# Kernel tuning notes

Measured on AMD Instinct MI355X. Metric: run time of the kernel, lower is better.

The kernel has to match this reference:

```python
import jax, jax.numpy as jnp
import numpy as np

LN_EPS = 1e-5
MASK_FILL = -1e9


def setup_inputs() -> dict:
    key = jax.random.key(0)
    ks = jax.random.split(key, 10)
    B, L, D, H, O, K = 128, 2048, 128, 256, 128, 64
    return {
        "sequence_emb": jax.random.normal(ks[0], (B, L, D), jnp.float32),
        "mask": jax.random.randint(ks[1], (B, L), 0, 2, jnp.int32),
        "target_emb": jax.random.normal(ks[2], (B, D), jnp.float32),
        "pos_table": jax.random.normal(ks[3], (10000, D), jnp.float32) * 0.02,
        "W_imp1": jax.random.normal(ks[4], (3 * D, H), jnp.float32) * (1.0 / np.sqrt(3 * D)),
        "b_imp1": jnp.zeros((H,), jnp.float32),
        "W_imp2": jax.random.normal(ks[5], (H, 1), jnp.float32) * (1.0 / np.sqrt(H)),
        "b_imp2": jnp.zeros((1,), jnp.float32),
        "W_enc1": jax.random.normal(ks[6], (2 * D, H), jnp.float32) * (1.0 / np.sqrt(2 * D)),
        "b_enc1": jnp.zeros((H,), jnp.float32),
        "W_enc2": jax.random.normal(ks[7], (H, O), jnp.float32) * (1.0 / np.sqrt(H)),
        "b_enc2": jnp.zeros((O,), jnp.float32),
        "ln_gamma": jnp.ones((O,), jnp.float32),
        "ln_beta": jnp.zeros((O,), jnp.float32),
        "top_k": K,
    }


def reference(sequence_emb, mask, target_emb, pos_table, W_imp1, b_imp1, W_imp2,
              b_imp2, W_enc1, b_enc1, W_enc2, b_enc2, ln_gamma, ln_beta, top_k):
    B, L, D = sequence_emb.shape
    # position embedding lookup (positions identical across batch -> keep (L,D) and broadcast)
    positions = jnp.minimum(jnp.arange(L), pos_table.shape[0] - 1)
    pos_emb = jnp.broadcast_to(pos_table[positions][None], (B, L, D))
    combined = jnp.concatenate([sequence_emb, pos_emb], axis=-1)          # (B,L,2D)
    tgt = jnp.broadcast_to(target_emb[:, None, :], (B, L, D))
    imp_in = jnp.concatenate([combined, tgt], axis=-1)                    # (B,L,3D)
    # importance MLP -> scalar score per event
    h = jax.nn.relu(imp_in @ W_imp1 + b_imp1)
    scores = (h @ W_imp2 + b_imp2)[..., 0]                                # (B,L)
    scores = jnp.where(mask == 0, MASK_FILL, scores)
    # masked top-k, then gather in chronological (sorted-index) order
    topk_values, topk_indices = jax.lax.top_k(scores, top_k)              # (B,K)
    idx_sorted = jnp.sort(topk_indices, axis=-1)
    sel = jnp.take_along_axis(combined, idx_sorted[..., None], axis=1)    # (B,K,2D)
    encoded = jax.nn.relu(sel @ W_enc1 + b_enc1) @ W_enc2 + b_enc2        # (B,K,O)
    # reorder scores to match sorted index order (torch: gather by argsort of indices)
    order = jnp.argsort(topk_indices, axis=-1)
    topk_scores = jnp.take_along_axis(topk_values, order, axis=-1)
    attn = jax.nn.softmax(topk_scores, axis=-1)                           # (B,K)
    pooled = jnp.einsum('bk,bkd->bd', attn, encoded)                      # (B,O)
    mu = jnp.mean(pooled, axis=-1, keepdims=True)
    var = jnp.var(pooled, axis=-1, keepdims=True)
    return (pooled - mu) * jax.lax.rsqrt(var + LN_EPS) * ln_gamma + ln_beta
```

## Files before the change

### kernel.cpp

```cpp
#include <hip/hip_runtime.h>
#include <hip/hip_bf16.h>

namespace {
constexpr int NB = 128;
constexpr int NL = 2048;
constexpr int ND = 128;
constexpr int NH = 256;
constexpr int NO = 128;
constexpr int NK = 64;
constexpr int MCAP = 192;
constexpr int HTHR = 96;
constexpr int BLOOP = 8;
constexpr float MASK_FILL_F = -1e9f;
constexpr float LN_EPS_F = 1e-5f;
}

typedef __attribute__((ext_vector_type(8))) short bf16x8;
typedef __attribute__((ext_vector_type(4))) float f32x4;

__device__ __forceinline__ unsigned short bf16rne(float x) {
  unsigned u = __float_as_uint(x);
  return (unsigned short)((u + 0x7FFFu + ((u >> 16) & 1u)) >> 16);
}

__global__ __launch_bounds__(256) void k_prep(
    const float* __restrict__ W1, const float* __restrict__ pos,
    const float* __restrict__ tgt, const float* __restrict__ b1,
    const float* __restrict__ We1, const float* __restrict__ We2,
    unsigned short* __restrict__ W1aT, float* __restrict__ P,
    float* __restrict__ T, unsigned short* __restrict__ We1T,
    unsigned short* __restrict__ We2T) {
  const int blk = blockIdx.x, t = threadIdx.x;
  if (blk < ND) {
    W1aT[(size_t)t * ND + blk] = bf16rne(W1[(size_t)blk * NH + t]);
    return;
  }
  if (blk >= ND + NL + NB) {
    const int b2 = blk - (ND + NL + NB);
    if (b2 < 256) {
      We1T[(size_t)t * 256 + b2] = bf16rne(We1[(size_t)b2 * NH + t]);
    } else {
      const int d = b2 - 256;
      if (t < NO) We2T[(size_t)t * 256 + d] = bf16rne(We2[(size_t)d * NO + t]);
    }
    return;
  }
  int r, w_off, add_bias;
  const float* src;
  float* out;
  if (blk < ND + NL) {
    r = blk - ND; src = pos; out = P; w_off = ND; add_bias = 1;
  } else {
    r = blk - (ND + NL); src = tgt; out = T; w_off = 2 * ND; add_bias = 0;
  }
  __shared__ float row[ND];
  if (t < ND) row[t] = src[(size_t)r * ND + t];
  __syncthreads();
  float acc = add_bias ? b1[t] : 0.0f;
#pragma unroll 8
  for (int d = 0; d < ND; ++d)
    acc = fmaf(row[d], W1[(size_t)(w_off + d) * NH + t], acc);
  out[(size_t)r * NH + t] = acc;
}

__global__ __launch_bounds__(512, 2) void k_scores_mfma(
    const float* __restrict__ seq, const int* __restrict__ mask,
    const unsigned short* __restrict__ W1aT, const float* __restrict__ w2,
    const float* __restrict__ b2, const float* __restrict__ b1,
    const float* __restrict__ T, float* __restrict__ scores) {
  const int l0 = blockIdx.x * 128;
  const int b0 = blockIdx.y * BLOOP;
  const int t = threadIdx.x;
  const int lane = t & 63;
  const int w = t >> 6;
  const int wh = w & 3;
  const int wl = w >> 2;
  const int lh = lane & 15;
  const int kq = lane >> 4;

  __shared__ unsigned short sSeq[2][128 * 128];
  __shared__ float sRed[4][128];

  bf16x8 a[4][4];
#pragma unroll
  for (int ks = 0; ks < 4; ++ks)
#pragma unroll
    for (int mt = 0; mt < 4; ++mt)
      a[ks][mt] = *(const bf16x8*)(
          W1aT + (size_t)(wh * 64 + mt * 16 + lh) * ND + ks * 32 + kq * 8);

  float4 wv[4], b1v[4];
#pragma unroll
  for (int mt = 0; mt < 4; ++mt) {
    wv[mt] = *(const float4*)(w2 + wh * 64 + mt * 16 + kq * 4);
    b1v[mt] = *(const float4*)(b1 + wh * 64 + mt * 16 + kq * 4);
  }
  const float b2v = b2[0];

  ushort4 pf[8];
  auto prefetch = [&](int bb) {
    const float4* g = (const float4*)(seq + ((size_t)bb * NL + l0) * ND);
#pragma unroll
    for (int i = 0; i < 8; ++i) {
      const float4 f = g[t + i * 512];
      pf[i].x = bf16rne(f.x); pf[i].y = bf16rne(f.y);
      pf[i].z = bf16rne(f.z); pf[i].w = bf16rne(f.w);
    }
  };
  auto commit = [&](unsigned short* dst) {
#pragma unroll
    for (int i = 0; i < 8; ++i) {
      const int v = t + i * 512;
      const int row = v >> 5;
      const int c8 = (v & 31) * 8;
      const int off = (row << 8) + (c8 ^ ((row & 15) << 4));
      *(ushort4*)((char*)dst + off) = pf[i];
    }
  };

  prefetch(b0);
  commit((unsigned short*)sSeq[0]);
  __syncthreads();

#pragma unroll 1
  for (int j = 0; j < BLOOP; ++j) {
    const int b = b0 + j;
    unsigned short* cSeq = (unsigned short*)sSeq[j & 1];
    unsigned short* nSeq = (unsigned short*)sSeq[(j & 1) ^ 1];

    if (j + 1 < BLOOP) prefetch(b + 1);

    float4 Tv[4];
#pragma unroll
    for (int mt = 0; mt < 4; ++mt)
      Tv[mt] = *(const float4*)(T + (size_t)b * NH + wh * 64 + mt * 16 + kq * 4);

    f32x4 acc[4][4];
#pragma unroll
    for (int mt = 0; mt < 4; ++mt)
#pragma unroll
      for (int nt = 0; nt < 4; ++nt) acc[mt][nt] = (f32x4){0.f, 0.f, 0.f, 0.f};

#pragma unroll
    for (int ks = 0; ks < 4; ++ks) {
      bf16x8 Bf[4];
#pragma unroll
      for (int nt = 0; nt < 4; ++nt) {
        const int row = wl * 64 + nt * 16 + lh;
        const int off = (row << 8) + (((ks << 6) + (kq << 4)) ^ ((row & 15) << 4));
        Bf[nt] = *(const bf16x8*)((const char*)cSeq + off);
      }
#pragma unroll
      for (int mt = 0; mt < 4; ++mt)
#pragma unroll
        for (int nt = 0; nt < 4; ++nt)
          acc[mt][nt] = __builtin_amdgcn_mfma_f32_16x16x32_bf16(
              a[ks][mt], Bf[nt], acc[mt][nt], 0, 0, 0);
    }
    __syncthreads();
    if (j + 1 < BLOOP) commit(nSeq);

    float p[4] = {0.f, 0.f, 0.f, 0.f};
#pragma unroll
    for (int mt = 0; mt < 4; ++mt) {
#pragma unroll
      for (int nt = 0; nt < 4; ++nt) {
        float z;
        z = acc[mt][nt][0] + Tv[mt].x + b1v[mt].x; p[nt] = fmaf(fmaxf(z, 0.f), wv[mt].x, p[nt]);
        z = acc[mt][nt][1] + Tv[mt].y + b1v[mt].y; p[nt] = fmaf(fmaxf(z, 0.f), wv[mt].y, p[nt]);
        z = acc[mt][nt][2] + Tv[mt].z + b1v[mt].z; p[nt] = fmaf(fmaxf(z, 0.f), wv[mt].z, p[nt]);
        z = acc[mt][nt][3] + Tv[mt].w + b1v[mt].w; p[nt] = fmaf(fmaxf(z, 0.f), wv[mt].w, p[nt]);
      }
    }
#pragma unroll
    for (int nt = 0; nt < 4; ++nt) {
      float v = p[nt];
      v += __shfl_xor(v, 16);
      v += __shfl_xor(v, 32);
      if (lane < 16) sRed[wh][wl * 64 + nt * 16 + lane] = v;
    }
    __syncthreads();
    if (t < 128) {
      const int l = l0 + t;
      float sc = sRed[0][t] + sRed[1][t] + sRed[2][t] + sRed[3][t] + b2v;
      if (mask[(size_t)b * NL + l] == 0) sc = MASK_FILL_F;
      scores[(size_t)b * NL + l] = sc;
    }
  }
}

__global__ __launch_bounds__(1024, 4) void k_topA(
    const float* __restrict__ scores, int* __restrict__ cand_idx,
    int* __restrict__ cand_n) {
  const int b = blockIdx.x, t = threadIdx.x;
  __shared__ unsigned hist[4096];
  __shared__ unsigned chunk[256];
  __shared__ unsigned suf[257];
  __shared__ int sCsel, sBsel;
  __shared__ unsigned sCntHi, sCntB;
  __shared__ int s_cand[MCAP];

  const unsigned mkey = ~__float_as_uint(MASK_FILL_F);
  for (int i = t; i < 4096; i += 1024) hist[i] = 0;
  if (t == 0) { sCntHi = 0; sCntB = 0; sCsel = 0; suf[256] = 0; }
  __syncthreads();
  unsigned key2[2];
#pragma unroll
  for (int i = 0; i < 2; ++i) {
    unsigned u = __float_as_uint(scores[(size_t)b * NL + t + i * 1024]);
    u = (u & 0x80000000u) ? ~u : (u | 0x80000000u);
    key2[i] = u;
    if (u != mkey) atomicAdd(&hist[u >> 20], 1u);
  }
  __syncthreads();
  if (t < 256) {
    unsigned s = 0;
#pragma unroll 4
    for (int j = 0; j < 16; ++j) s += hist[t * 16 + j];
    chunk[t] = s;
  }
  __syncthreads();
  if (t < 256) {
    unsigned s = 0;
    for (int j = t; j < 256; ++j) s += chunk[j];
    suf[t] = s;
    if (s >= (unsigned)HTHR) atomicMax(&sCsel, t);
  }
  __syncthreads();
  const int c = sCsel;
  if (t == 0) sBsel = c * 16;
  __syncthreads();
  if (t < 16) {
    unsigned s = 0;
    for (int j = c * 16 + t; j < c * 16 + 16; ++j) s += hist[j];
    if (s + suf[c + 1] >= (unsigned)HTHR) atomicMax(&sBsel, c * 16 + t);
  }
  __syncthreads();
  const unsigned B = (unsigned)sBsel;
#pragma unroll
  for (int i = 0; i < 2; ++i) {
    if (key2[i] != mkey && (key2[i] >> 20) > B) {
      unsigned pos_ = atomicAdd(&sCntHi, 1u);
      s_cand[pos_] = t + i * 1024;
    }
  }
  __syncthreads();
  const unsigned hi = sCntHi;
#pragma unroll
  for (int i = 0; i < 2; ++i) {
    if (key2[i] != mkey && (key2[i] >> 20) == B) {
      unsigned pos_ = atomicAdd(&sCntB, 1u);
      if (hi + pos_ < (unsigned)MCAP) s_cand[hi + pos_] = t + i * 1024;
    }
  }
  __syncthreads();
  unsigned n = sCntHi + sCntB;
  if (n > (unsigned)MCAP) n = MCAP;
  if (t < MCAP) cand_idx[(size_t)b * MCAP + t] = (t < (int)n) ? s_cand[t] : 0;
  if (t == 0) cand_n[b] = (int)n;
}

__global__ __launch_bounds__(256) void k_rescoreW(
    const float* __restrict__ seq, const int* __restrict__ mask,
    const float* __restrict__ W1, const float* __restrict__ w2,
    const float* __restrict__ b2, const float* __restrict__ P,
    const float* __restrict__ T, const int* __restrict__ cand_idx,
    const int* __restrict__ cand_n, float* __restrict__ cscore) {
  const int b = blockIdx.y;
  const int s0 = blockIdx.x * 32;
  const int n = cand_n[b];
  if (s0 >= n) return;
  const int t = threadIdx.x;
  __shared__ float s_seq[32 * 128];
  __shared__ int s_l[32];
  if (t < 32) {
    const int slot = s0 + t;
    s_l[t] = (slot < n) ? cand_idx[(size_t)b * MCAP + slot] : 0;
  }
  __syncthreads();
#pragma unroll
  for (int i = 0; i < 4; ++i) {
    const int v = t + i * 256;
    const int r = v >> 5, c = v & 31;
    ((float4*)s_seq)[r * 32 + c] =
        ((const float4*)(seq + ((size_t)b * NL + s_l[r]) * ND))[c];
  }
  __syncthreads();

  const int hg = t & 63, rg = t >> 6;
  float acc[8][4];
#pragma unroll
  for (int r = 0; r < 8; ++r)
#pragma unroll
    for (int j = 0; j < 4; ++j) acc[r][j] = 0.0f;

  const float4* Wp = (const float4*)W1;
  for (int d0 = 0; d0 < ND; d0 += 4) {
    float4 wq[4];
#pragma unroll
    for (int j = 0; j < 4; ++j) wq[j] = Wp[(size_t)(d0 + j) * (NH / 4) + hg];
#pragma unroll
    for (int r = 0; r < 8; ++r) {
      const float4 s = *(const float4*)&s_seq[(rg * 8 + r) * ND + d0];
      const float sv[4] = {s.x, s.y, s.z, s.w};
#pragma unroll
      for (int j = 0; j < 4; ++j) {
        acc[r][0] = fmaf(sv[j], wq[j].x, acc[r][0]);
        acc[r][1] = fmaf(sv[j], wq[j].y, acc[r][1]);
        acc[r][2] = fmaf(sv[j], wq[j].z, acc[r][2]);
        acc[r][3] = fmaf(sv[j], wq[j].w, acc[r][3]);
      }
    }
  }

  const float4 wv = ((const float4*)w2)[hg];
  const float4 Tv = ((const float4*)(T + (size_t)b * NH))[hg];
  const float b2v = b2[0];
#pragma unroll
  for (int r = 0; r < 8; ++r) {
    const int l = s_l[rg * 8 + r];
    const float4 Pv = ((const float4*)(P + (size_t)l * NH))[hg];
    float z, p = 0.0f;
    z = acc[r][0] + Pv.x + Tv.x; p = fmaf(fmaxf(z, 0.0f), wv.x, p);
    z = acc[r][1] + Pv.y + Tv.y; p = fmaf(fmaxf(z, 0.0f), wv.y, p);
    z = acc[r][2] + Pv.z + Tv.z; p = fmaf(fmaxf(z, 0.0f), wv.z, p);
    z = acc[r][3] + Pv.w + Tv.w; p = fmaf(fmaxf(z, 0.0f), wv.w, p);
#pragma unroll
    for (int off = 32; off >= 1; off >>= 1) p += __shfl_xor(p, off);
    if (hg == 0) {
      float sc = p + b2v;
      if (mask[(size_t)b * NL + l] == 0) sc = MASK_FILL_F;
      cscore[(size_t)b * MCAP + s0 + rg * 8 + r] = sc;
    }
  }
}

__global__ __launch_bounds__(512, 2) void k_selenc(
    const float* __restrict__ cscore, const int* __restrict__ cand_idx,
    const int* __restrict__ cand_n, const float* __restrict__ seq,
    const float* __restrict__ pos,
    const unsigned short* __restrict__ We1T, const float* __restrict__ be1,
    const unsigned short* __restrict__ We2T, const float* __restrict__ be2,
    const float* __restrict__ gamma, const float* __restrict__ beta,
    float* __restrict__ out) {
  const int b = blockIdx.x, t = threadIdx.x;
  const int lane = t & 63, w = t >> 6;
  const int lh = lane & 15, kq = lane >> 4;
  __shared__ unsigned long long s_key[MCAP];
  __shared__ float s_cs[MCAP];
  __shared__ int sel_l[NK];
  __shared__ float sel_v[NK];
  __shared__ int srt_l[NK];
  __shared__ float srt_v[NK];
  __shared__ float s_at[NK];
  __shared__ unsigned short s_in[64 * 256];
  __shared__ unsigned short s_h1[64 * 256];
  __shared__ float red[4][128];
  __shared__ float rr[4];

  const int n = cand_n[b];
  for (int s = t; s < MCAP; s += 512) {
    unsigned long long kk = 0ull;
    float f = 0.0f;
    if (s < n) {
      f = cscore[(size_t)b * MCAP + s];
      unsigned u = __float_as_uint(f);
      u = (u & 0x80000000u) ? ~u : (u | 0x80000000u);
      const int l = cand_idx[(size_t)b * MCAP + s];
      kk = ((unsigned long long)u << 11) | (unsigned long long)(NL - 1 - l);
    }
    s_key[s] = kk;
    s_cs[s] = f;
  }
  __syncthreads();
  for (int s = t; s < MCAP; s += 512) {
    if (s < n) {
      const unsigned long long mk = s_key[s];
      int rank = 0;
      for (int j = 0; j < n; ++j) rank += (s_key[j] > mk) ? 1 : 0;
      if (rank < NK) {
        sel_l[rank] = (NL - 1) - (int)(mk & 0x7FFull);
        sel_v[rank] = s_cs[s];
      }
    }
  }
  __syncthreads();
  if (t < NK) {
    const int myl = sel_l[t];
    int pos_ = 0;
#pragma unroll 8
    for (int j = 0; j < NK; ++j) pos_ += (sel_l[j] < myl) ? 1 : 0;
    srt_l[pos_] = myl;
    srt_v[pos_] = sel_v[t];
  }
  __syncthreads();
  if (t < 64) {
    const float sc = srt_v[t];
    float m = sc;
#pragma unroll
    for (int off = 32; off >= 1; off >>= 1) m = fmaxf(m, __shfl_xor(m, off));
    const float e = expf(sc - m);
    float s = e;
#pragma unroll
    for (int off = 32; off >= 1; off >>= 1) s += __shfl_xor(s, off);
    s_at[t] = e / s;
  }
  __syncthreads();

#pragma unroll
  for (int i = 0; i < 8; ++i) {
    const int v = t + i * 512;
    const int row = v >> 6;
    const int q = v & 63;
    const int idx = srt_l[row];
    float4 f;
    if (q < 32) f = ((const float4*)(seq + ((size_t)b * NL + idx) * ND))[q];
    else        f = ((const float4*)(pos + (size_t)idx * ND))[q - 32];
    ushort4 hv;
    hv.x = bf16rne(f.x); hv.y = bf16rne(f.y);
    hv.z = bf16rne(f.z); hv.w = bf16rne(f.w);
    const int off = (row << 9) + ((q * 8) ^ ((row & 15) << 4));
    *(ushort4*)((char*)s_in + off) = hv;
  }
  __syncthreads();

  {
    const int wh = w & 3, wn = w >> 2;
    f32x4 acc1[4][2];
#pragma unroll
    for (int mt = 0; mt < 4; ++mt)
#pragma unroll
      for (int nt = 0; nt < 2; ++nt) acc1[mt][nt] = (f32x4){0.f, 0.f, 0.f, 0.f};
#pragma unroll
    for (int ks = 0; ks < 8; ++ks) {
      bf16x8 Bf[2];
#pragma unroll
      for (int nt = 0; nt < 2; ++nt) {
        const int row = wn * 32 + nt * 16 + lh;
        const int off = (row << 9) + ((ks * 64 + kq * 16) ^ ((row & 15) << 4));
        Bf[nt] = *(const bf16x8*)((const char*)s_in + off);
      }
#pragma unroll
      for (int mt = 0; mt < 4; ++mt) {
        const bf16x8 Af = *(const bf16x8*)(
            We1T + (size_t)(wh * 64 + mt * 16 + lh) * 256 + ks * 32 + kq * 8);
#pragma unroll
        for (int nt = 0; nt < 2; ++nt)
          acc1[mt][nt] = __builtin_amdgcn_mfma_f32_16x16x32_bf16(
              Af, Bf[nt], acc1[mt][nt], 0, 0, 0);
      }
    }
#pragma unroll
    for (int mt = 0; mt < 4; ++mt) {
      const int h0 = wh * 64 + mt * 16 + kq * 4;
      const float4 bv = *(const float4*)(be1 + h0);
#pragma unroll
      for (int nt = 0; nt < 2; ++nt) {
        const int row = wn * 32 + nt * 16 + lh;
        const float z0 = fmaxf(acc1[mt][nt][0] + bv.x, 0.0f);
        const float z1 = fmaxf(acc1[mt][nt][1] + bv.y, 0.0f);
        const float z2 = fmaxf(acc1[mt][nt][2] + bv.z, 0.0f);
        const float z3 = fmaxf(acc1[mt][nt][3] + bv.w, 0.0f);
        const unsigned u0 = (unsigned)bf16rne(z0) | ((unsigned)bf16rne(z1) << 16);
        const unsigned u1 = (unsigned)bf16rne(z2) | ((unsigned)bf16rne(z3) << 16);
        const int off = (row << 9) + ((h0 * 2) ^ ((row & 15) << 4));
        *(unsigned*)((char*)s_h1 + off) = u0;
        *(unsigned*)((char*)s_h1 + off + 4) = u1;
      }
    }
  }
  __syncthreads();

  {
    const int wo = w & 1, wn4 = w >> 1;
    const int row = wn4 * 16 + lh;
    f32x4 acc2[4];
#pragma unroll
    for (int mt = 0; mt < 4; ++mt) acc2[mt] = (f32x4){0.f, 0.f, 0.f, 0.f};
#pragma unroll
    for (int ks = 0; ks < 8; ++ks) {
      const int off = (row << 9) + ((ks * 64 + kq * 16) ^ ((row & 15) << 4));
      const bf16x8 Bf = *(const bf16x8*)((const char*)s_h1 + off);
#pragma unroll
      for (int mt = 0; mt < 4; ++mt) {
        const bf16x8 Af = *(const bf16x8*)(
            We2T + (size_t)(wo * 64 + mt * 16 + lh) * 256 + ks * 32 + kq * 8);
        acc2[mt] = __builtin_amdgcn_mfma_f32_16x16x32_bf16(Af, Bf, acc2[mt], 0, 0, 0);
      }
    }
    const float at = s_at[row];
#pragma unroll
    for (int mt = 0; mt < 4; ++mt) {
#pragma unroll
      for (int j = 0; j < 4; ++j) {
        float v = acc2[mt][j] * at;
        v += __shfl_xor(v, 1);
        v += __shfl_xor(v, 2);
        v += __shfl_xor(v, 4);
        v += __shfl_xor(v, 8);
        if (lh == 0) red[wn4][wo * 64 + mt * 16 + kq * 4 + j] = v;
      }
    }
  }
  __syncthreads();

  float pooled = 0.0f;
  if (t < NO)
    pooled = red[0][t] + red[1][t] + red[2][t] + red[3][t] + be2[t];
  float s1 = (t < NO) ? pooled : 0.0f;
  float s2 = (t < NO) ? pooled * pooled : 0.0f;
#pragma unroll
  for (int off = 32; off >= 1; off >>= 1) {
    s1 += __shfl_xor(s1, off);
    s2 += __shfl_xor(s2, off);
  }
  if (t < NO && (t & 63) == 0) {
    rr[(t >> 6) * 2] = s1;
    rr[(t >> 6) * 2 + 1] = s2;
  }
  __syncthreads();
  if (t < NO) {
    const float S1 = rr[0] + rr[2];
    const float S2 = rr[1] + rr[3];
    const float mu = S1 / NO;
    const float var = S2 / NO - mu * mu;
    const float rs = rsqrtf(var + LN_EPS_F);
    out[(size_t)b * NO + t] = (pooled - mu) * rs * gamma[t] + beta[t];
  }
}

extern "C" void kernel_launch(void* const* d_in, const int* in_sizes, int n_in,
                              void* d_out, int out_size, void* d_ws, size_t ws_size,
                              hipStream_t stream) {
  (void)in_sizes; (void)n_in; (void)out_size; (void)ws_size;
  const float* seq = (const float*)d_in[0];
  const int* mask = (const int*)d_in[1];
  const float* tgt = (const float*)d_in[2];
  const float* pos = (const float*)d_in[3];
  const float* W1 = (const float*)d_in[4];
  const float* b1 = (const float*)d_in[5];
  const float* w2 = (const float*)d_in[6];
  const float* b2 = (const float*)d_in[7];
  const float* We1 = (const float*)d_in[8];
  const float* be1 = (const float*)d_in[9];
  const float* We2 = (const float*)d_in[10];
  const float* be2 = (const float*)d_in[11];
  const float* gam = (const float*)d_in[12];
  const float* bet = (const float*)d_in[13];
  float* out = (float*)d_out;

  float* P = (float*)d_ws;
  float* T = P + (size_t)NL * NH;
  float* scores = T + (size_t)NB * NH;
  unsigned short* w1aT = (unsigned short*)(scores + (size_t)NB * NL);
  unsigned short* we1T = w1aT + (size_t)NH * ND;
  unsigned short* we2T = we1T + (size_t)256 * 256;
  int* cand_idx = (int*)(we2T + (size_t)128 * 256);
  int* cand_n = cand_idx + (size_t)NB * MCAP;
  float* cscore = (float*)(cand_n + NB);

  k_prep<<<ND + NL + NB + 512, 256, 0, stream>>>(W1, pos, tgt, b1, We1, We2,
                                                 w1aT, P, T, we1T, we2T);
  k_scores_mfma<<<dim3(NL / 128, NB / BLOOP), 512, 0, stream>>>(
      seq, mask, w1aT, w2, b2, b1, T, scores);
  k_topA<<<NB, 1024, 0, stream>>>(scores, cand_idx, cand_n);
  k_rescoreW<<<dim3(MCAP / 32, NB), 256, 0, stream>>>(
      seq, mask, W1, w2, b2, P, T, cand_idx, cand_n, cscore);
  k_selenc<<<NB, 512, 0, stream>>>(cscore, cand_idx, cand_n, seq, pos,
                                   we1T, be1, we2T, be2, gam, bet, out);
}
```

Measured before the change: 116.5 us.

## Fuse top-k candidate, rescore and encode stages into one cooperative kernel

```diff
diff --git a/kernel.cpp b/kernel.cpp
--- a/kernel.cpp
+++ b/kernel.cpp
@@ -1,5 +1,8 @@
 #include <hip/hip_runtime.h>
 #include <hip/hip_bf16.h>
+#include <hip/hip_cooperative_groups.h>
+
+namespace cg = cooperative_groups;
 
 namespace {
 constexpr int NB = 128;
@@ -189,343 +192,347 @@
   }
 }
 
-__global__ __launch_bounds__(1024, 4) void k_topA(
-    const float* __restrict__ scores, int* __restrict__ cand_idx,
-    int* __restrict__ cand_n) {
-  const int b = blockIdx.x, t = threadIdx.x;
-  __shared__ unsigned hist[4096];
-  __shared__ unsigned chunk[256];
-  __shared__ unsigned suf[257];
-  __shared__ int sCsel, sBsel;
-  __shared__ unsigned sCntHi, sCntB;
-  __shared__ int s_cand[MCAP];
-
-  const unsigned mkey = ~__float_as_uint(MASK_FILL_F);
-  for (int i = t; i < 4096; i += 1024) hist[i] = 0;
-  if (t == 0) { sCntHi = 0; sCntB = 0; sCsel = 0; suf[256] = 0; }
-  __syncthreads();
-  unsigned key2[2];
-#pragma unroll
-  for (int i = 0; i < 2; ++i) {
-    unsigned u = __float_as_uint(scores[(size_t)b * NL + t + i * 1024]);
-    u = (u & 0x80000000u) ? ~u : (u | 0x80000000u);
-    key2[i] = u;
-    if (u != mkey) atomicAdd(&hist[u >> 20], 1u);
-  }
-  __syncthreads();
-  if (t < 256) {
-    unsigned s = 0;
-#pragma unroll 4
-    for (int j = 0; j < 16; ++j) s += hist[t * 16 + j];
-    chunk[t] = s;
-  }
-  __syncthreads();
-  if (t < 256) {
-    unsigned s = 0;
-    for (int j = t; j < 256; ++j) s += chunk[j];
-    suf[t] = s;
-    if (s >= (unsigned)HTHR) atomicMax(&sCsel, t);
-  }
-  __syncthreads();
-  const int c = sCsel;
-  if (t == 0) sBsel = c * 16;
-  __syncthreads();
-  if (t < 16) {
-    unsigned s = 0;
-    for (int j = c * 16 + t; j < c * 16 + 16; ++j) s += hist[j];
-    if (s + suf[c + 1] >= (unsigned)HTHR) atomicMax(&sBsel, c * 16 + t);
-  }
-  __syncthreads();
-  const unsigned B = (unsigned)sBsel;
-#pragma unroll
-  for (int i = 0; i < 2; ++i) {
-    if (key2[i] != mkey && (key2[i] >> 20) > B) {
-      unsigned pos_ = atomicAdd(&sCntHi, 1u);
-      s_cand[pos_] = t + i * 1024;
-    }
-  }
-  __syncthreads();
-  const unsigned hi = sCntHi;
-#pragma unroll
-  for (int i = 0; i < 2; ++i) {
-    if (key2[i] != mkey && (key2[i] >> 20) == B) {
-      unsigned pos_ = atomicAdd(&sCntB, 1u);
-      if (hi + pos_ < (unsigned)MCAP) s_cand[hi + pos_] = t + i * 1024;
-    }
-  }
-  __syncthreads();
-  unsigned n = sCntHi + sCntB;
-  if (n > (unsigned)MCAP) n = MCAP;
-  if (t < MCAP) cand_idx[(size_t)b * MCAP + t] = (t < (int)n) ? s_cand[t] : 0;
-  if (t == 0) cand_n[b] = (int)n;
-}
-
-__global__ __launch_bounds__(256) void k_rescoreW(
-    const float* __restrict__ seq, const int* __restrict__ mask,
-    const float* __restrict__ W1, const float* __restrict__ w2,
-    const float* __restrict__ b2, const float* __restrict__ P,
-    const float* __restrict__ T, const int* __restrict__ cand_idx,
-    const int* __restrict__ cand_n, float* __restrict__ cscore) {
-  const int b = blockIdx.y;
-  const int s0 = blockIdx.x * 32;
-  const int n = cand_n[b];
-  if (s0 >= n) return;
-  const int t = threadIdx.x;
-  __shared__ float s_seq[32 * 128];
-  __shared__ int s_l[32];
-  if (t < 32) {
-    const int slot = s0 + t;
-    s_l[t] = (slot < n) ? cand_idx[(size_t)b * MCAP + slot] : 0;
-  }
-  __syncthreads();
-#pragma unroll
-  for (int i = 0; i < 4; ++i) {
-    const int v = t + i * 256;
-    const int r = v >> 5, c = v & 31;
-    ((float4*)s_seq)[r * 32 + c] =
-        ((const float4*)(seq + ((size_t)b * NL + s_l[r]) * ND))[c];
-  }
-  __syncthreads();
-
-  const int hg = t & 63, rg = t >> 6;
-  float acc[8][4];
-#pragma unroll
-  for (int r = 0; r < 8; ++r)
-#pragma unroll
-    for (int j = 0; j < 4; ++j) acc[r][j] = 0.0f;
-
-  const float4* Wp = (const float4*)W1;
-  for (int d0 = 0; d0 < ND; d0 += 4) {
-    float4 wq[4];
-#pragma unroll
-    for (int j = 0; j < 4; ++j) wq[j] = Wp[(size_t)(d0 + j) * (NH / 4) + hg];
-#pragma unroll
-    for (int r = 0; r < 8; ++r) {
-      const float4 s = *(const float4*)&s_seq[(rg * 8 + r) * ND + d0];
-      const float sv[4] = {s.x, s.y, s.z, s.w};
-#pragma unroll
-      for (int j = 0; j < 4; ++j) {
-        acc[r][0] = fmaf(sv[j], wq[j].x, acc[r][0]);
-        acc[r][1] = fmaf(sv[j], wq[j].y, acc[r][1]);
-        acc[r][2] = fmaf(sv[j], wq[j].z, acc[r][2]);
-        acc[r][3] = fmaf(sv[j], wq[j].w, acc[r][3]);
-      }
-    }
-  }
-
-  const float4 wv = ((const float4*)w2)[hg];
-  const float4 Tv = ((const float4*)(T + (size_t)b * NH))[hg];
-  const float b2v = b2[0];
-#pragma unroll
-  for (int r = 0; r < 8; ++r) {
-    const int l = s_l[rg * 8 + r];
-    const float4 Pv = ((const float4*)(P + (size_t)l * NH))[hg];
-    float z, p = 0.0f;
-    z = acc[r][0] + Pv.x + Tv.x; p = fmaf(fmaxf(z, 0.0f), wv.x, p);
-    z = acc[r][1] + Pv.y + Tv.y; p = fmaf(fmaxf(z, 0.0f), wv.y, p);
-    z = acc[r][2] + Pv.z + Tv.z; p = fmaf(fmaxf(z, 0.0f), wv.z, p);
-    z = acc[r][3] + Pv.w + Tv.w; p = fmaf(fmaxf(z, 0.0f), wv.w, p);
-#pragma unroll
-    for (int off = 32; off >= 1; off >>= 1) p += __shfl_xor(p, off);
-    if (hg == 0) {
-      float sc = p + b2v;
-      if (mask[(size_t)b * NL + l] == 0) sc = MASK_FILL_F;
-      cscore[(size_t)b * MCAP + s0 + rg * 8 + r] = sc;
-    }
-  }
-}
-
-__global__ __launch_bounds__(512, 2) void k_selenc(
-    const float* __restrict__ cscore, const int* __restrict__ cand_idx,
-    const int* __restrict__ cand_n, const float* __restrict__ seq,
+__global__ __launch_bounds__(512, 2) void k_tail_coop(
+    const float* __restrict__ scores, const float* __restrict__ seq,
+    const int* __restrict__ mask, const float* __restrict__ W1,
+    const float* __restrict__ w2, const float* __restrict__ b2,
+    const float* __restrict__ P, const float* __restrict__ T,
     const float* __restrict__ pos,
     const unsigned short* __restrict__ We1T, const float* __restrict__ be1,
     const unsigned short* __restrict__ We2T, const float* __restrict__ be2,
     const float* __restrict__ gamma, const float* __restrict__ beta,
-    float* __restrict__ out) {
-  const int b = blockIdx.x, t = threadIdx.x;
+    int* __restrict__ cand_idx, int* __restrict__ cand_n,
+    float* __restrict__ cscore, float* __restrict__ out) {
+  cg::grid_group grid = cg::this_grid();
+  const int blk = blockIdx.x, t = threadIdx.x;
   const int lane = t & 63, w = t >> 6;
   const int lh = lane & 15, kq = lane >> 4;
-  __shared__ unsigned long long s_key[MCAP];
-  __shared__ float s_cs[MCAP];
+
+  __shared__ __align__(16) char smem[71680];
+  __shared__ int sCsel, sBsel;
+  __shared__ unsigned sCntHi, sCntB;
+  __shared__ int s_candA[MCAP];
   __shared__ int sel_l[NK];
   __shared__ float sel_v[NK];
   __shared__ int srt_l[NK];
   __shared__ float srt_v[NK];
   __shared__ float s_at[NK];
-  __shared__ unsigned short s_in[64 * 256];
-  __shared__ unsigned short s_h1[64 * 256];
   __shared__ float red[4][128];
   __shared__ float rr[4];
 
-  const int n = cand_n[b];
-  for (int s = t; s < MCAP; s += 512) {
-    unsigned long long kk = 0ull;
-    float f = 0.0f;
-    if (s < n) {
-      f = cscore[(size_t)b * MCAP + s];
-      unsigned u = __float_as_uint(f);
+  if (blk < NB) {
+    const int b = blk;
+    unsigned* hist = (unsigned*)smem;
+    unsigned* chunk = hist + 4096;
+    unsigned* suf = chunk + 256;
+    const unsigned mkey = ~__float_as_uint(MASK_FILL_F);
+    for (int i = t; i < 4096; i += 512) hist[i] = 0;
+    if (t == 0) { sCntHi = 0; sCntB = 0; sCsel = 0; suf[256] = 0; }
+    __syncthreads();
+    unsigned key4[4];
+#pragma unroll
+    for (int i = 0; i < 4; ++i) {
+      unsigned u = __float_as_uint(scores[(size_t)b * NL + t + i * 512]);
       u = (u & 0x80000000u) ? ~u : (u | 0x80000000u);
-      const int l = cand_idx[(size_t)b * MCAP + s];
-      kk = ((unsigned long long)u << 11) | (unsigned long long)(NL - 1 - l);
-    }
-    s_key[s] = kk;
-    s_cs[s] = f;
-  }
-  __syncthreads();
-  for (int s = t; s < MCAP; s += 512) {
-    if (s < n) {
-      const unsigned long long mk = s_key[s];
-      int rank = 0;
-      for (int j = 0; j < n; ++j) rank += (s_key[j] > mk) ? 1 : 0;
-      if (rank < NK) {
-        sel_l[rank] = (NL - 1) - (int)(mk & 0x7FFull);
-        sel_v[rank] = s_cs[s];
-      }
-    }
-  }
-  __syncthreads();
-  if (t < NK) {
-    const int myl = sel_l[t];
-    int pos_ = 0;
+      key4[i] = u;
+      if (u != mkey) atomicAdd(&hist[u >> 20], 1u);
+    }
+    __syncthreads();
+    if (t < 256) {
+      unsigned s = 0;
+#pragma unroll 4
+      for (int j = 0; j < 16; ++j) s += hist[t * 16 + j];
+      chunk[t] = s;
+    }
+    __syncthreads();
+    if (t < 256) {
+      unsigned s = 0;
+      for (int j = t; j < 256; ++j) s += chunk[j];
+      suf[t] = s;
+      if (s >= (unsigned)HTHR) atomicMax(&sCsel, t);
+    }
+    __syncthreads();
+    const int c = sCsel;
+    if (t == 0) sBsel = c * 16;
+    __syncthreads();
+    if (t < 16) {
+      unsigned s = 0;
+      for (int j = c * 16 + t; j < c * 16 + 16; ++j) s += hist[j];
+      if (s + suf[c + 1] >= (unsigned)HTHR) atomicMax(&sBsel, c * 16 + t);
+    }
+    __syncthreads();
+    const unsigned B = (unsigned)sBsel;
+#pragma unroll
+    for (int i = 0; i < 4; ++i) {
+      if (key4[i] != mkey && (key4[i] >> 20) > B) {
+        unsigned pos_ = atomicAdd(&sCntHi, 1u);
+        s_candA[pos_] = t + i * 512;
+      }
+    }
+    __syncthreads();
+    const unsigned hi = sCntHi;
+#pragma unroll
+    for (int i = 0; i < 4; ++i) {
+      if (key4[i] != mkey && (key4[i] >> 20) == B) {
+        unsigned pos_ = atomicAdd(&sCntB, 1u);
+        if (hi + pos_ < (unsigned)MCAP) s_candA[hi + pos_] = t + i * 512;
+      }
+    }
+    __syncthreads();
+    unsigned n = sCntHi + sCntB;
+    if (n > (unsigned)MCAP) n = MCAP;
+    if (t < MCAP) cand_idx[(size_t)b * MCAP + t] = (t < (int)n) ? s_candA[t] : 0;
+    if (t == 0) cand_n[b] = (int)n;
+  }
+  grid.sync();
+
+  {
+    const int b = blk >> 1;
+    const int base = (blk & 1) * 96;
+    const int n = cand_n[b];
+    if (base < n) {
+      float* s_stage = (float*)smem;
+      int* s_l = (int*)(smem + 96 * ND * 4);
+      if (t < 96)
+        s_l[t] = (base + t < n) ? cand_idx[(size_t)b * MCAP + base + t] : 0;
+      __syncthreads();
+#pragma unroll
+      for (int i = 0; i < 6; ++i) {
+        const int v = t + i * 512;
+        const int r = v >> 5, cc = v & 31;
+        ((float4*)s_stage)[v] =
+            ((const float4*)(seq + ((size_t)b * NL + s_l[r]) * ND))[cc];
+      }
+      __syncthreads();
+
+      const int hg = lane;
+      const int rg = w;
+      const float4* Wp = (const float4*)W1;
+      const float4 wvq = ((const float4*)w2)[hg];
+      const float4 Tvq = ((const float4*)(T + (size_t)b * NH))[hg];
+      const float b2v = b2[0];
+      float acc[12][4];
+#pragma unroll
+      for (int r = 0; r < 12; ++r)
+#pragma unroll
+        for (int j = 0; j < 4; ++j) acc[r][j] = 0.0f;
+
+      for (int d0 = 0; d0 < ND; d0 += 4) {
+        float4 wq[4];
+#pragma unroll
+        for (int j = 0; j < 4; ++j) wq[j] = Wp[(size_t)(d0 + j) * (NH / 4) + hg];
+#pragma unroll
+        for (int r = 0; r < 12; ++r) {
+          const float4 s = *(const float4*)&s_stage[(rg * 12 + r) * ND + d0];
+          const float sv[4] = {s.x, s.y, s.z, s.w};
+#pragma unroll
+          for (int j = 0; j < 4; ++j) {
+            acc[r][0] = fmaf(sv[j], wq[j].x, acc[r][0]);
+            acc[r][1] = fmaf(sv[j], wq[j].y, acc[r][1]);
+            acc[r][2] = fmaf(sv[j], wq[j].z, acc[r][2]);
+            acc[r][3] = fmaf(sv[j], wq[j].w, acc[r][3]);
+          }
+        }
+      }
+
+#pragma unroll
+      for (int r = 0; r < 12; ++r) {
+        const int l = s_l[rg * 12 + r];
+        const float4 Pv = ((const float4*)(P + (size_t)l * NH))[hg];
+        float z, p = 0.0f;
+        z = acc[r][0] + Pv.x + Tvq.x; p = fmaf(fmaxf(z, 0.0f), wvq.x, p);
+        z = acc[r][1] + Pv.y + Tvq.y; p = fmaf(fmaxf(z, 0.0f), wvq.y, p);
+        z = acc[r][2] + Pv.z + Tvq.z; p = fmaf(fmaxf(z, 0.0f), wvq.z, p);
+        z = acc[r][3] + Pv.w + Tvq.w; p = fmaf(fmaxf(z, 0.0f), wvq.w, p);
+#pragma unroll
+        for (int off = 32; off >= 1; off >>= 1) p += __shfl_xor(p, off);
+        if (hg == 0) {
+          float sc = p + b2v;
+          if (mask[(size_t)b * NL + l] == 0) sc = MASK_FILL_F;
+          cscore[(size_t)b * MCAP + base + rg * 12 + r] = sc;
+        }
+      }
+    }
+  }
+  grid.sync();
+
+  if (blk >= NB) return;
+  {
+    const int b = blk;
+    unsigned long long* s_key = (unsigned long long*)smem;
+    float* s_cs = (float*)(smem + MCAP * 8);
+    unsigned short* s_in = (unsigned short*)(smem + 4096);
+    unsigned short* s_h1 = (unsigned short*)(smem + 4096 + 32768);
+
+    const int n = cand_n[b];
+    for (int s = t; s < MCAP; s += 512) {
+      unsigned long long kk = 0ull;
+      float f = 0.0f;
+      if (s < n) {
+        f = cscore[(size_t)b * MCAP + s];
+        unsigned u = __float_as_uint(f);
+        u = (u & 0x80000000u) ? ~u : (u | 0x80000000u);
+        const int l = cand_idx[(size_t)b * MCAP + s];
+        kk = ((unsigned long long)u << 11) | (unsigned long long)(NL - 1 - l);
+      }
+      s_key[s] = kk;
+      s_cs[s] = f;
+    }
+    __syncthreads();
+    for (int s = t; s < MCAP; s += 512) {
+      if (s < n) {
+        const unsigned long long mk = s_key[s];
+        int rank = 0;
+        for (int j = 0; j < n; ++j) rank += (s_key[j] > mk) ? 1 : 0;
+        if (rank < NK) {
+          sel_l[rank] = (NL - 1) - (int)(mk & 0x7FFull);
+          sel_v[rank] = s_cs[s];
+        }
+      }
+    }
+    __syncthreads();
+    if (t < NK) {
+      const int myl = sel_l[t];
+      int pos_ = 0;
 #pragma unroll 8
-    for (int j = 0; j < NK; ++j) pos_ += (sel_l[j] < myl) ? 1 : 0;
-    srt_l[pos_] = myl;
-    srt_v[pos_] = sel_v[t];
-  }
-  __syncthreads();
-  if (t < 64) {
-    const float sc = srt_v[t];
-    float m = sc;
-#pragma unroll
-    for (int off = 32; off >= 1; off >>= 1) m = fmaxf(m, __shfl_xor(m, off));
-    const float e = expf(sc - m);
-    float s = e;
-#pragma unroll
-    for (int off = 32; off >= 1; off >>= 1) s += __shfl_xor(s, off);
-    s_at[t] = e / s;
-  }
-  __syncthreads();
-
-#pragma unroll
-  for (int i = 0; i < 8; ++i) {
-    const int v = t + i * 512;
-    const int row = v >> 6;
-    const int q = v & 63;
-    const int idx = srt_l[row];
-    float4 f;
-    if (q < 32) f = ((const float4*)(seq + ((size_t)b * NL + idx) * ND))[q];
-    else        f = ((const float4*)(pos + (size_t)idx * ND))[q - 32];
-    ushort4 hv;
-    hv.x = bf16rne(f.x); hv.y = bf16rne(f.y);
-    hv.z = bf16rne(f.z); hv.w = bf16rne(f.w);
-    const int off = (row << 9) + ((q * 8) ^ ((row & 15) << 4));
-    *(ushort4*)((char*)s_in + off) = hv;
-  }
-  __syncthreads();
-
-  {
-    const int wh = w & 3, wn = w >> 2;
-    f32x4 acc1[4][2];
-#pragma unroll
-    for (int mt = 0; mt < 4; ++mt)
-#pragma unroll
-      for (int nt = 0; nt < 2; ++nt) acc1[mt][nt] = (f32x4){0.f, 0.f, 0.f, 0.f};
-#pragma unroll
-    for (int ks = 0; ks < 8; ++ks) {
-      bf16x8 Bf[2];
-#pragma unroll
-      for (int nt = 0; nt < 2; ++nt) {
-        const int row = wn * 32 + nt * 16 + lh;
+      for (int j = 0; j < NK; ++j) pos_ += (sel_l[j] < myl) ? 1 : 0;
+      srt_l[pos_] = myl;
+      srt_v[pos_] = sel_v[t];
+    }
+    __syncthreads();
+    if (t < 64) {
+      const float sc = srt_v[t];
+      float m = sc;
+#pragma unroll
+      for (int off = 32; off >= 1; off >>= 1) m = fmaxf(m, __shfl_xor(m, off));
+      const float e = expf(sc - m);
+      float s = e;
+#pragma unroll
+      for (int off = 32; off >= 1; off >>= 1) s += __shfl_xor(s, off);
+      s_at[t] = e / s;
+    }
+    __syncthreads();
+
+#pragma unroll
+    for (int i = 0; i < 8; ++i) {
+      const int v = t + i * 512;
+      const int row = v >> 6;
+      const int q = v & 63;
+      const int idx = srt_l[row];
+      float4 f;
+      if (q < 32) f = ((const float4*)(seq + ((size_t)b * NL + idx) * ND))[q];
+      else        f = ((const float4*)(pos + (size_t)idx * ND))[q - 32];
+      ushort4 hv;
+      hv.x = bf16rne(f.x); hv.y = bf16rne(f.y);
+      hv.z = bf16rne(f.z); hv.w = bf16rne(f.w);
+      const int off = (row << 9) + ((q * 8) ^ ((row & 15) << 4));
+      *(ushort4*)((char*)s_in + off) = hv;
+    }
+    __syncthreads();
+
+    {
+      const int wh = w & 3, wn = w >> 2;
+      f32x4 acc1[4][2];
+#pragma unroll
+      for (int mt = 0; mt < 4; ++mt)
+#pragma unroll
+        for (int nt = 0; nt < 2; ++nt) acc1[mt][nt] = (f32x4){0.f, 0.f, 0.f, 0.f};
+#pragma unroll
+      for (int ks = 0; ks < 8; ++ks) {
+        bf16x8 Bf[2];
+#pragma unroll
+        for (int nt = 0; nt < 2; ++nt) {
+          const int row = wn * 32 + nt * 16 + lh;
+          const int off = (row << 9) + ((ks * 64 + kq * 16) ^ ((row & 15) << 4));
+          Bf[nt] = *(const bf16x8*)((const char*)s_in + off);
+        }
+#pragma unroll
+        for (int mt = 0; mt < 4; ++mt) {
+          const bf16x8 Af = *(const bf16x8*)(
+              We1T + (size_t)(wh * 64 + mt * 16 + lh) * 256 + ks * 32 + kq * 8);
+#pragma unroll
+          for (int nt = 0; nt < 2; ++nt)
+            acc1[mt][nt] = __builtin_amdgcn_mfma_f32_16x16x32_bf16(
+                Af, Bf[nt], acc1[mt][nt], 0, 0, 0);
+        }
+      }
+#pragma unroll
+      for (int mt = 0; mt < 4; ++mt) {
+        const int h0 = wh * 64 + mt * 16 + kq * 4;
+        const float4 bv = *(const float4*)(be1 + h0);
+#pragma unroll
+        for (int nt = 0; nt < 2; ++nt) {
+          const int row = wn * 32 + nt * 16 + lh;
+          const float z0 = fmaxf(acc1[mt][nt][0] + bv.x, 0.0f);
+          const float z1 = fmaxf(acc1[mt][nt][1] + bv.y, 0.0f);
+          const float z2 = fmaxf(acc1[mt][nt][2] + bv.z, 0.0f);
+          const float z3 = fmaxf(acc1[mt][nt][3] + bv.w, 0.0f);
+          const unsigned u0 = (unsigned)bf16rne(z0) | ((unsigned)bf16rne(z1) << 16);
+          const unsigned u1 = (unsigned)bf16rne(z2) | ((unsigned)bf16rne(z3) << 16);
+          const int off = (row << 9) + ((h0 * 2) ^ ((row & 15) << 4));
+          *(unsigned*)((char*)s_h1 + off) = u0;
+          *(unsigned*)((char*)s_h1 + off + 4) = u1;
+        }
+      }
+    }
+    __syncthreads();
+
+    {
+      const int wo = w & 1, wn4 = w >> 1;
+      const int row = wn4 * 16 + lh;
+      f32x4 acc2[4];
+#pragma unroll
+      for (int mt = 0; mt < 4; ++mt) acc2[mt] = (f32x4){0.f, 0.f, 0.f, 0.f};
+#pragma unroll
+      for (int ks = 0; ks < 8; ++ks) {
         const int off = (row << 9) + ((ks * 64 + kq * 16) ^ ((row & 15) << 4));
-        Bf[nt] = *(const bf16x8*)((const char*)s_in + off);
-      }
+        const bf16x8 Bf = *(const bf16x8*)((const char*)s_h1 + off);
+#pragma unroll
+        for (int mt = 0; mt < 4; ++mt) {
+          const bf16x8 Af = *(const bf16x8*)(
+              We2T + (size_t)(wo * 64 + mt * 16 + lh) * 256 + ks * 32 + kq * 8);
+          acc2[mt] = __builtin_amdgcn_mfma_f32_16x16x32_bf16(Af, Bf, acc2[mt], 0, 0, 0);
+        }
+      }
+      const float at = s_at[row];
 #pragma unroll
       for (int mt = 0; mt < 4; ++mt) {
-        const bf16x8 Af = *(const bf16x8*)(
-            We1T + (size_t)(wh * 64 + mt * 16 + lh) * 256 + ks * 32 + kq * 8);
-#pragma unroll
-        for (int nt = 0; nt < 2; ++nt)
-          acc1[mt][nt] = __builtin_amdgcn_mfma_f32_16x16x32_bf16(
-              Af, Bf[nt], acc1[mt][nt], 0, 0, 0);
-      }
-    }
-#pragma unroll
-    for (int mt = 0; mt < 4; ++mt) {
-      const int h0 = wh * 64 + mt * 16 + kq * 4;
-      const float4 bv = *(const float4*)(be1 + h0);
-#pragma unroll
-      for (int nt = 0; nt < 2; ++nt) {
-        const int row = wn * 32 + nt * 16 + lh;
-        const float z0 = fmaxf(acc1[mt][nt][0] + bv.x, 0.0f);
-        const float z1 = fmaxf(acc1[mt][nt][1] + bv.y, 0.0f);
-        const float z2 = fmaxf(acc1[mt][nt][2] + bv.z, 0.0f);
-        const float z3 = fmaxf(acc1[mt][nt][3] + bv.w, 0.0f);
-        const unsigned u0 = (unsigned)bf16rne(z0) | ((unsigned)bf16rne(z1) << 16);
-        const unsigned u1 = (unsigned)bf16rne(z2) | ((unsigned)bf16rne(z3) << 16);
-        const int off = (row << 9) + ((h0 * 2) ^ ((row & 15) << 4));
-        *(unsigned*)((char*)s_h1 + off) = u0;
-        *(unsigned*)((char*)s_h1 + off + 4) = u1;
-      }
-    }
-  }
-  __syncthreads();
-
-  {
-    const int wo = w & 1, wn4 = w >> 1;
-    const int row = wn4 * 16 + lh;
-    f32x4 acc2[4];
-#pragma unroll
-    for (int mt = 0; mt < 4; ++mt) acc2[mt] = (f32x4){0.f, 0.f, 0.f, 0.f};
-#pragma unroll
-    for (int ks = 0; ks < 8; ++ks) {
-      const int off = (row << 9) + ((ks * 64 + kq * 16) ^ ((row & 15) << 4));
-      const bf16x8 Bf = *(const bf16x8*)((const char*)s_h1 + off);
-#pragma unroll
-      for (int mt = 0; mt < 4; ++mt) {
-        const bf16x8 Af = *(const bf16x8*)(
-            We2T + (size_t)(wo * 64 + mt * 16 + lh) * 256 + ks * 32 + kq * 8);
-        acc2[mt] = __builtin_amdgcn_mfma_f32_16x16x32_bf16(Af, Bf, acc2[mt], 0, 0, 0);
-      }
-    }
-    const float at = s_at[row];
-#pragma unroll
-    for (int mt = 0; mt < 4; ++mt) {
-#pragma unroll
-      for (int j = 0; j < 4; ++j) {
-        float v = acc2[mt][j] * at;
-        v += __shfl_xor(v, 1);
-        v += __shfl_xor(v, 2);
-        v += __shfl_xor(v, 4);
-        v += __shfl_xor(v, 8);
-        if (lh == 0) red[wn4][wo * 64 + mt * 16 + kq * 4 + j] = v;
-      }
-    }
-  }
-  __syncthreads();
-
-  float pooled = 0.0f;
-  if (t < NO)
-    pooled = red[0][t] + red[1][t] + red[2][t] + red[3][t] + be2[t];
-  float s1 = (t < NO) ? pooled : 0.0f;
-  float s2 = (t < NO) ? pooled * pooled : 0.0f;
-#pragma unroll
-  for (int off = 32; off >= 1; off >>= 1) {
-    s1 += __shfl_xor(s1, off);
-    s2 += __shfl_xor(s2, off);
-  }
-  if (t < NO && (t & 63) == 0) {
-    rr[(t >> 6) * 2] = s1;
-    rr[(t >> 6) * 2 + 1] = s2;
-  }
-  __syncthreads();
-  if (t < NO) {
-    const float S1 = rr[0] + rr[2];
-    const float S2 = rr[1] + rr[3];
-    const float mu = S1 / NO;
-    const float var = S2 / NO - mu * mu;
-    const float rs = rsqrtf(var + LN_EPS_F);
-    out[(size_t)b * NO + t] = (pooled - mu) * rs * gamma[t] + beta[t];
+#pragma unroll
+        for (int j = 0; j < 4; ++j) {
+          float v = acc2[mt][j] * at;
+          v += __shfl_xor(v, 1);
+          v += __shfl_xor(v, 2);
+          v += __shfl_xor(v, 4);
+          v += __shfl_xor(v, 8);
+          if (lh == 0) red[wn4][wo * 64 + mt * 16 + kq * 4 + j] = v;
+        }
+      }
+    }
+    __syncthreads();
+
+    float pooled = 0.0f;
+    if (t < NO)
+      pooled = red[0][t] + red[1][t] + red[2][t] + red[3][t] + be2[t];
+    float s1 = (t < NO) ? pooled : 0.0f;
+    float s2 = (t < NO) ? pooled * pooled : 0.0f;
+#pragma unroll
+    for (int off = 32; off >= 1; off >>= 1) {
+      s1 += __shfl_xor(s1, off);
+      s2 += __shfl_xor(s2, off);
+    }
+    if (t < NO && (t & 63) == 0) {
+      rr[(t >> 6) * 2] = s1;
+      rr[(t >> 6) * 2 + 1] = s2;
+    }
+    __syncthreads();
+    if (t < NO) {
+      const float S1 = rr[0] + rr[2];
+      const float S2 = rr[1] + rr[3];
+      const float mu = S1 / NO;
+      const float var = S2 / NO - mu * mu;
+      const float rs = rsqrtf(var + LN_EPS_F);
+      out[(size_t)b * NO + t] = (pooled - mu) * rs * gamma[t] + beta[t];
+    }
   }
 }
 
@@ -563,9 +570,12 @@
                                                  w1aT, P, T, we1T, we2T);
   k_scores_mfma<<<dim3(NL / 128, NB / BLOOP), 512, 0, stream>>>(
       seq, mask, w1aT, w2, b2, b1, T, scores);
-  k_topA<<<NB, 1024, 0, stream>>>(scores, cand_idx, cand_n);
-  k_rescoreW<<<dim3(MCAP / 32, NB), 256, 0, stream>>>(
-      seq, mask, W1, w2, b2, P, T, cand_idx, cand_n, cscore);
-  k_selenc<<<NB, 512, 0, stream>>>(cscore, cand_idx, cand_n, seq, pos,
-                                   we1T, be1, we2T, be2, gam, bet, out);
+
+  void* args[] = {
+      (void*)&scores, (void*)&seq, (void*)&mask, (void*)&W1, (void*)&w2,
+      (void*)&b2, (void*)&P, (void*)&T, (void*)&pos, (void*)&we1T,
+      (void*)&be1, (void*)&we2T, (void*)&be2, (void*)&gam, (void*)&bet,
+      (void*)&cand_idx, (void*)&cand_n, (void*)&cscore, (void*)&out};
+  hipLaunchCooperativeKernel((void*)k_tail_coop, dim3(256), dim3(512), args, 0,
+                             stream);
 }
```

Measured after the change: 176.7 us. +51.7%, slower.
